# Optimization experiments

Hardware: AMD Instinct MI355X
Metric: run time of the kernel (lower is better)

## Reference

```python
import jax, jax.numpy as jnp
import numpy as np

# LinearMoELayer(input_size=2048, output_size=2048, num_experts=8, num_selects=2,
#                bias=True, gate_network='mlp', gate_use_balance=True,
#                gate_add_noise=True, gate_use_softmax=True)
# Eval-mode forward semantics (deterministic: noise branch only active in training).
B, S, D, O, E, K = 4, 2048, 2048, 2048, 8, 2
BAL_W = 1e-2   # balance_loss_weight
EPS = 1e-10    # cv_squared eps


def setup_inputs() -> dict:
    key = jax.random.key(0)
    ks = jax.random.split(key, 5)
    x = jax.random.normal(ks[0], (B, S, D), dtype=jnp.float32)
    # gate 'mlp': Linear(D,E,bias=False) -> tanh -> Linear(E,E,bias=False)
    gate_w1 = jax.random.normal(ks[1], (E, D), dtype=jnp.float32) * (1.0 / np.sqrt(D))
    gate_w2 = jax.random.normal(ks[2], (E, E), dtype=jnp.float32) * (1.0 / np.sqrt(E))
    # LinearExperts: per-expert weight [E, O, D] and bias [E, O] (F.linear convention)
    expert_w = jax.random.normal(ks[3], (E, O, D), dtype=jnp.float32) * (1.0 / np.sqrt(D))
    expert_b = jax.random.normal(ks[4], (E, O), dtype=jnp.float32) * 0.01
    return {"x": x, "gate_w1": gate_w1, "gate_w2": gate_w2,
            "expert_w": expert_w, "expert_b": expert_b}


def _cv_squared(v):
    # torch: v.var() / (v.mean()**2 + eps); torch.var is unbiased (ddof=1)
    m = jnp.mean(v)
    var = jnp.sum((v - m) ** 2) / (v.shape[0] - 1)
    return var / (m * m + EPS)


def reference(x, gate_w1, gate_w2, expert_w, expert_b):
    xt = x.reshape(-1, D)                                  # [T, D]
    T = xt.shape[0]
    # --- TopKBalancedNoisyGate (eval path) ---
    logits = jnp.tanh(xt @ gate_w1.T) @ gate_w2.T          # [T, E]
    top_logits, top_idx = jax.lax.top_k(logits, K)         # [T, K]
    scores = jax.nn.softmax(top_logits.astype(jnp.float32), axis=-1)  # [T, K]
    # scatter top-k scores into dense [T, E] gate matrix
    dense = jnp.zeros((T, E), dtype=scores.dtype)
    dense = dense.at[jnp.arange(T)[:, None], top_idx].set(scores)
    importance = dense.sum(axis=0)                         # [E]
    load = (dense > 0).sum(axis=0).astype(jnp.float32)     # [E] token counts
    gate_loss = BAL_W * (_cv_squared(importance) + _cv_squared(load))
    # --- UniversalCalculator: per-expert linear + score-weighted combine ---
    # math-equivalent to sort/dispatch/grouped-linear/index_add combine
    h = jnp.einsum('td,eod->teo', xt, expert_w) + expert_b[None, :, :]  # [T, E, O]
    y = jnp.einsum('te,teo->to', dense, h)                 # [T, O]
    return y.reshape(B, S, O), gate_loss
```

## Files before the change

kernel.cpp:

```cpp
#include <hip/hip_runtime.h>
#include <hip/hip_bf16.h>

#define TT 8192
#define DD 2048
#define OO 2048
#define EE 8

typedef __attribute__((ext_vector_type(4))) float f32x4;
typedef __attribute__((ext_vector_type(8))) short s16x8;
typedef __attribute__((ext_vector_type(4))) short s16x4;

__device__ __forceinline__ short f2bf(float f) {
    union { float f; unsigned u; } v; v.f = f;
    unsigned r = (v.u + 0x7FFFu + ((v.u >> 16) & 1u)) >> 16;
    return (short)(unsigned short)r;
}
__device__ __forceinline__ float bf2f(short s) {
    union { unsigned u; float f; } v; v.u = ((unsigned)(unsigned short)s) << 16;
    return v.f;
}

__global__ __launch_bounds__(256) void cvt_bf16_kernel(const float* __restrict__ in,
                                                       short* __restrict__ out, long n8) {
    long i = (long)blockIdx.x * blockDim.x + threadIdx.x;
    long stride = (long)gridDim.x * blockDim.x;
    for (; i < n8; i += stride) {
        f32x4 a = ((const f32x4*)in)[i * 2];
        f32x4 b = ((const f32x4*)in)[i * 2 + 1];
        s16x8 r;
        r[0] = f2bf(a[0]); r[1] = f2bf(a[1]); r[2] = f2bf(a[2]); r[3] = f2bf(a[3]);
        r[4] = f2bf(b[0]); r[5] = f2bf(b[1]); r[6] = f2bf(b[2]); r[7] = f2bf(b[3]);
        ((s16x8*)out)[i] = r;
    }
}

__global__ __launch_bounds__(256) void gate_kernel(
    const float* __restrict__ x, const float* __restrict__ w1, const float* __restrict__ w2,
    int* __restrict__ tk_idx, float* __restrict__ tk_score)
{
    const int lane = threadIdx.x & 63;
    const int wid = threadIdx.x >> 6;
    const int t = blockIdx.x * 4 + wid;
    const float* xt = x + (long)t * DD;

    float acc[8] = {0.f,0.f,0.f,0.f,0.f,0.f,0.f,0.f};
#pragma unroll
    for (int i = 0; i < DD / 256; ++i) {
        f32x4 xv = *(const f32x4*)&xt[i * 256 + lane * 4];
#pragma unroll
        for (int e2 = 0; e2 < 8; ++e2) {
            f32x4 wv = *(const f32x4*)&w1[e2 * DD + i * 256 + lane * 4];
            acc[e2] += xv[0]*wv[0] + xv[1]*wv[1] + xv[2]*wv[2] + xv[3]*wv[3];
        }
    }
#pragma unroll
    for (int e2 = 0; e2 < 8; ++e2) {
#pragma unroll
        for (int off = 32; off > 0; off >>= 1)
            acc[e2] += __shfl_xor(acc[e2], off, 64);
    }

    float th[8], lg[8];
#pragma unroll
    for (int e2 = 0; e2 < 8; ++e2) th[e2] = tanhf(acc[e2]);
#pragma unroll
    for (int eo = 0; eo < 8; ++eo) {
        float s = 0.f;
#pragma unroll
        for (int e2 = 0; e2 < 8; ++e2) s += th[e2] * w2[eo * 8 + e2];
        lg[eo] = s;
    }
    int e0 = 0;
#pragma unroll
    for (int q = 1; q < 8; ++q) if (lg[q] > lg[e0]) e0 = q;
    int e1 = (e0 == 0) ? 1 : 0;
#pragma unroll
    for (int q = 0; q < 8; ++q) if (q != e0 && lg[q] > lg[e1]) e1 = q;

    float d = expf(lg[e1] - lg[e0]);
    float s0 = 1.f / (1.f + d);
    float s1 = d / (1.f + d);

    if (lane == 0) {
        tk_idx[t * 2] = e0; tk_idx[t * 2 + 1] = e1;
        tk_score[t * 2] = s0; tk_score[t * 2 + 1] = s1;
    }
}

__global__ __launch_bounds__(256) void build_lists(
    const int* __restrict__ tk_idx, const float* __restrict__ tk_score,
    int* __restrict__ tok_list, float* __restrict__ score_list, int* __restrict__ cnt,
    float* __restrict__ imp)
{
    const int e = blockIdx.x;
    const int lane = threadIdx.x & 63;
    const int wid = threadIdx.x >> 6;
    __shared__ int wsum[4];
    __shared__ float wsumF[4];
    int base = 0;
    float ssum = 0.f;
    for (int t0 = 0; t0 < TT; t0 += 256) {
        int t = t0 + threadIdx.x;
        int i0 = tk_idx[t * 2], i1 = tk_idx[t * 2 + 1];
        bool has = (i0 == e) || (i1 == e);
        int slot = (i0 == e) ? 0 : 1;
        float sc = (i0 == e) ? tk_score[t * 2] : tk_score[t * 2 + 1];
        unsigned long long m = __ballot(has);
        int prefix = __popcll(m & ((1ull << lane) - 1ull));
        if (lane == 0) wsum[wid] = __popcll(m);
        __syncthreads();
        int woff = 0;
#pragma unroll
        for (int w = 0; w < 4; ++w) woff += (w < wid) ? wsum[w] : 0;
        int total = wsum[0] + wsum[1] + wsum[2] + wsum[3];
        if (has) {
            int p = base + woff + prefix;
            tok_list[e * TT + p] = t * 2 + slot;
            score_list[e * TT + p] = sc;
            ssum += sc;
        }
        base += total;
        __syncthreads();
    }
#pragma unroll
    for (int off = 32; off > 0; off >>= 1)
        ssum += __shfl_xor(ssum, off, 64);
    if (lane == 0) wsumF[wid] = ssum;
    __syncthreads();
    if (threadIdx.x == 0) {
        cnt[e] = base;
        imp[e] = wsumF[0] + wsumF[1] + wsumF[2] + wsumF[3];
    }
}

__global__ __launch_bounds__(64) void loss_finalize(const float* __restrict__ imp,
                                                    const int* __restrict__ cnt,
                                                    float* __restrict__ loss_out)
{
    if (threadIdx.x == 0) {
        float im[8], ld[8];
        float mi = 0.f, ml = 0.f;
#pragma unroll
        for (int q = 0; q < 8; ++q) {
            im[q] = imp[q]; ld[q] = (float)cnt[q];
            mi += im[q]; ml += ld[q];
        }
        mi *= 0.125f; ml *= 0.125f;
        float vi = 0.f, vl = 0.f;
#pragma unroll
        for (int q = 0; q < 8; ++q) {
            float a = im[q] - mi; vi += a * a;
            float b = ld[q] - ml; vl += b * b;
        }
        vi /= 7.f; vl /= 7.f;
        loss_out[0] = 0.01f * (vi / (mi * mi + 1e-10f) + vl / (ml * ml + 1e-10f));
    }
}

__global__ __launch_bounds__(256) void combine_kernel(float* __restrict__ y,
                                                      const short* __restrict__ part1) {
    long i = (long)blockIdx.x * blockDim.x + threadIdx.x;
    long stride = (long)gridDim.x * blockDim.x;
    const long n4 = (long)TT * OO / 4;
    for (; i < n4; i += stride) {
        f32x4 v = ((const f32x4*)y)[i];
        s16x4 p = ((const s16x4*)part1)[i];
        v[0] += bf2f(p[0]); v[1] += bf2f(p[1]);
        v[2] += bf2f(p[2]); v[3] += bf2f(p[3]);
        ((f32x4*)y)[i] = v;
    }
}

#define GLD16(gsrc, ldst) \
    __builtin_amdgcn_global_load_lds((const __attribute__((address_space(1))) unsigned int*)(gsrc), \
                                     (__attribute__((address_space(3))) unsigned int*)(ldst), 16, 0, 0)

#define BAR() __builtin_amdgcn_s_barrier()

__global__ __launch_bounds__(512, 2) void moe_gemm(
    const short* __restrict__ xbf, const short* __restrict__ wbf,
    const float* __restrict__ eb,
    const int* __restrict__ tok_list, const float* __restrict__ score_list,
    const int* __restrict__ cnt, float* __restrict__ y, short* __restrict__ part1)
{
    const int e = blockIdx.z;
    const int n_e = cnt[e];
    const int row0 = blockIdx.y * 256;
    if (row0 >= n_e) return;
    const int col0 = blockIdx.x * 256;

    __shared__ alignas(16) short lds[2 * 32768];
    __shared__ int   stok[256];
    __shared__ float ssc[256];

    const int tid = threadIdx.x;
    const int lane = tid & 63;
    const int wid = tid >> 6;
    const int wr = wid >> 2, wc = wid & 3;
    const int fr = lane & 15, fq = lane >> 4;
    const char* ldsb = (const char*)lds;

    if (tid < 256) {
        int slot = row0 + tid;
        if (slot >= n_e) slot = n_e - 1;
        stok[tid] = tok_list[e * TT + slot];
        ssc[tid]  = score_list[e * TT + slot];
    }
    __syncthreads();

    const int r_ = tid >> 3;
    const int csw = ((tid & 7) ^ (r_ & 7)) * 8;
    const short* aS[4];
#pragma unroll
    for (int g = 0; g < 4; ++g)
        aS[g] = xbf + (long)(stok[g * 64 + r_] >> 1) * DD + csw;
    const short* bS[4];
#pragma unroll
    for (int g = 0; g < 4; ++g)
        bS[g] = wbf + (long)e * OO * DD + (long)(col0 + g * 64 + r_) * DD + csw;

#define STAGE_A(g, kt) GLD16(aS[g] + (kt) * 64, (char*)lds + ((kt) & 1) * 65536 + ((g) * 512 + tid) * 16)
#define STAGE_B(g, kt) GLD16(bS[g] + (kt) * 64, (char*)lds + ((kt) & 1) * 65536 + 32768 + ((g) * 512 + tid) * 16)

    const int aBase = (wr * 128 + fr) * 128;
    const int bBase = 32768 + (wc * 64 + fr) * 128;
    const int sw0 = (fq ^ (fr & 7)) * 16;
    const int sw1 = ((fq + 4) ^ (fr & 7)) * 16;

    f32x4 acc[8][4];
#pragma unroll
    for (int m = 0; m < 8; ++m)
#pragma unroll
        for (int n = 0; n < 4; ++n) acc[m][n] = f32x4{0.f, 0.f, 0.f, 0.f};

    STAGE_A(0, 0); STAGE_A(1, 0); STAGE_A(2, 0); STAGE_A(3, 0);
    STAGE_B(0, 0); STAGE_B(1, 0); STAGE_B(2, 0); STAGE_B(3, 0);
    STAGE_A(0, 1); STAGE_A(1, 1);
    asm volatile("s_waitcnt vmcnt(2)");
    BAR();

#pragma unroll 1
    for (int j = 0; j < DD / 64; ++j) {
        const int fb = (j & 1) * 65536;
        const bool st1 = (j + 1) < DD / 64;
        const bool st2 = (j + 2) < DD / 64;

        s16x8 a0[4][2], a1[4][2], bb[4][2];

#pragma unroll
        for (int mm = 0; mm < 4; ++mm) {
            a0[mm][0] = *(const s16x8*)(ldsb + fb + aBase + mm * 2048 + sw0);
            a0[mm][1] = *(const s16x8*)(ldsb + fb + aBase + mm * 2048 + sw1);
        }
#pragma unroll
        for (int n = 0; n < 4; ++n) {
            bb[n][0] = *(const s16x8*)(ldsb + fb + bBase + n * 2048 + sw0);
            bb[n][1] = *(const s16x8*)(ldsb + fb + bBase + n * 2048 + sw1);
        }
        if (st1) {
            STAGE_A(2, j + 1); STAGE_A(3, j + 1);
            STAGE_B(0, j + 1); STAGE_B(1, j + 1);
            STAGE_B(2, j + 1); STAGE_B(3, j + 1);
        }
#pragma unroll
        for (int mm = 0; mm < 4; ++mm)
#pragma unroll
            for (int n = 0; n < 4; ++n) {
                acc[mm][n] = __builtin_amdgcn_mfma_f32_16x16x32_bf16(a0[mm][0], bb[n][0], acc[mm][n], 0, 0, 0);
                acc[mm][n] = __builtin_amdgcn_mfma_f32_16x16x32_bf16(a0[mm][1], bb[n][1], acc[mm][n], 0, 0, 0);
            }
#pragma unroll
        for (int mm = 0; mm < 4; ++mm) {
            a1[mm][0] = *(const s16x8*)(ldsb + fb + aBase + 8192 + mm * 2048 + sw0);
            a1[mm][1] = *(const s16x8*)(ldsb + fb + aBase + 8192 + mm * 2048 + sw1);
        }
#pragma unroll
        for (int mm = 0; mm < 4; ++mm)
#pragma unroll
            for (int n = 0; n < 4; ++n) {
                acc[4 + mm][n] = __builtin_amdgcn_mfma_f32_16x16x32_bf16(a1[mm][0], bb[n][0], acc[4 + mm][n], 0, 0, 0);
                acc[4 + mm][n] = __builtin_amdgcn_mfma_f32_16x16x32_bf16(a1[mm][1], bb[n][1], acc[4 + mm][n], 0, 0, 0);
            }

        BAR();
        if (st2) { STAGE_A(0, j + 2); STAGE_A(1, j + 2); }
        if (st2) { asm volatile("s_waitcnt vmcnt(2)"); }
        else     { asm volatile("s_waitcnt vmcnt(0)"); }
        BAR();
    }

    float bval[4];
#pragma unroll
    for (int n = 0; n < 4; ++n)
        bval[n] = eb[e * OO + col0 + wc * 64 + n * 16 + fr];

#pragma unroll
    for (int m = 0; m < 8; ++m) {
#pragma unroll
        for (int jj = 0; jj < 4; ++jj) {
            int tslot = wr * 128 + m * 16 + fq * 4 + jj;
            if (row0 + tslot < n_e) {
                int packed = stok[tslot];
                int t = packed >> 1;
                float s = ssc[tslot];
                if ((packed & 1) == 0) {
#pragma unroll
                    for (int n = 0; n < 4; ++n) {
                        int o = col0 + wc * 64 + n * 16 + fr;
                        y[(long)t * OO + o] = s * (acc[m][n][jj] + bval[n]);
                    }
                } else {
#pragma unroll
                    for (int n = 0; n < 4; ++n) {
                        int o = col0 + wc * 64 + n * 16 + fr;
                        part1[(long)t * OO + o] = f2bf(s * (acc[m][n][jj] + bval[n]));
                    }
                }
            }
        }
    }
#undef STAGE_A
#undef STAGE_B
}

extern "C" void kernel_launch(void* const* d_in, const int* in_sizes, int n_in,
                              void* d_out, int out_size, void* d_ws, size_t ws_size,
                              hipStream_t stream) {
    const float* x  = (const float*)d_in[0];
    const float* w1 = (const float*)d_in[1];
    const float* w2 = (const float*)d_in[2];
    const float* ew = (const float*)d_in[3];
    const float* eb = (const float*)d_in[4];
    float* y = (float*)d_out;

    char* ws = (char*)d_ws;
    short* xbf = (short*)ws;            ws += (size_t)TT * DD * 2;
    short* wbf = (short*)ws;            ws += (size_t)EE * OO * DD * 2;
    short* part1 = (short*)ws;          ws += (size_t)TT * OO * 2;
    int*   tok_list = (int*)ws;         ws += (size_t)EE * TT * 4;
    float* score_list = (float*)ws;     ws += (size_t)EE * TT * 4;
    int*   tk_idx = (int*)ws;           ws += (size_t)TT * 2 * 4;
    float* tk_score = (float*)ws;       ws += (size_t)TT * 2 * 4;
    int*   cnt = (int*)ws;              ws += 64;
    float* imp = (float*)ws;            ws += 64;

    cvt_bf16_kernel<<<4096, 256, 0, stream>>>(ew, wbf, (long)EE * OO * DD / 8);
    cvt_bf16_kernel<<<2048, 256, 0, stream>>>(x,  xbf, (long)TT * DD / 8);
    gate_kernel<<<TT / 4, 256, 0, stream>>>(x, w1, w2, tk_idx, tk_score);
    build_lists<<<EE, 256, 0, stream>>>(tk_idx, tk_score, tok_list, score_list, cnt, imp);
    loss_finalize<<<1, 64, 0, stream>>>(imp, cnt, y + (size_t)TT * OO);
    moe_gemm<<<dim3(OO / 256, TT / 256, EE), 512, 0, stream>>>(
        xbf, wbf, eb, tok_list, score_list, cnt, y, part1);
    combine_kernel<<<2048, 256, 0, stream>>>(y, part1);
}
```

Baseline: 333.5 us.

## Switch MoE GEMM to triple-buffered K=32 LDS pipeline with one barrier per step

Reworks the expert GEMM main loop from a double-buffered K=64 tile with two barriers per iteration into a three-stage ring of K=32 tiles. Each stage is prefetched two iterations ahead and a single barrier is issued per step. LDS use drops from 128KB to 96KB per block, and the swizzle is adjusted for 64-byte rows. The goal is deeper overlap of global-to-LDS loads with MFMA work and less barrier stall. The cost is twice as many loop iterations, with smaller per-iteration MFMA batches and more frequent waits.

```diff
diff --git a/kernel.cpp b/kernel.cpp
--- a/kernel.cpp
+++ b/kernel.cpp
@@ -189,7 +189,7 @@
     if (row0 >= n_e) return;
     const int col0 = blockIdx.x * 256;
 
-    __shared__ alignas(16) short lds[2 * 32768];
+    __shared__ alignas(16) short lds[3 * 16384];
     __shared__ int   stok[256];
     __shared__ float ssc[256];
 
@@ -208,24 +208,27 @@
     }
     __syncthreads();
 
-    const int r_ = tid >> 3;
-    const int csw = ((tid & 7) ^ (r_ & 7)) * 8;
-    const short* aS[4];
-#pragma unroll
-    for (int g = 0; g < 4; ++g)
-        aS[g] = xbf + (long)(stok[g * 64 + r_] >> 1) * DD + csw;
-    const short* bS[4];
-#pragma unroll
-    for (int g = 0; g < 4; ++g)
-        bS[g] = wbf + (long)e * OO * DD + (long)(col0 + g * 64 + r_) * DD + csw;
-
-#define STAGE_A(g, kt) GLD16(aS[g] + (kt) * 64, (char*)lds + ((kt) & 1) * 65536 + ((g) * 512 + tid) * 16)
-#define STAGE_B(g, kt) GLD16(bS[g] + (kt) * 64, (char*)lds + ((kt) & 1) * 65536 + 32768 + ((g) * 512 + tid) * 16)
-
-    const int aBase = (wr * 128 + fr) * 128;
-    const int bBase = 32768 + (wc * 64 + fr) * 128;
-    const int sw0 = (fq ^ (fr & 7)) * 16;
-    const int sw1 = ((fq + 4) ^ (fr & 7)) * 16;
+    const int r4 = tid >> 2;
+    const int csw = ((tid & 3) ^ (r4 & 3)) * 8;
+    const short* aS[2];
+#pragma unroll
+    for (int g = 0; g < 2; ++g)
+        aS[g] = xbf + (long)(stok[g * 128 + r4] >> 1) * DD + csw;
+    const short* bS[2];
+#pragma unroll
+    for (int g = 0; g < 2; ++g)
+        bS[g] = wbf + (long)e * OO * DD + (long)(col0 + g * 128 + r4) * DD + csw;
+
+#define STAGE(kt, fb2) do { \
+    GLD16(aS[0] + (kt) * 32, (char*)lds + (fb2) + tid * 16);                 \
+    GLD16(aS[1] + (kt) * 32, (char*)lds + (fb2) + 8192 + tid * 16);          \
+    GLD16(bS[0] + (kt) * 32, (char*)lds + (fb2) + 16384 + tid * 16);         \
+    GLD16(bS[1] + (kt) * 32, (char*)lds + (fb2) + 16384 + 8192 + tid * 16);  \
+} while (0)
+
+    const int aBase = (wr * 128 + fr) * 64;
+    const int bBase = 16384 + (wc * 64 + fr) * 64;
+    const int sw = (fq ^ (fr & 3)) * 16;
 
     f32x4 acc[8][4];
 #pragma unroll
@@ -233,60 +236,38 @@
 #pragma unroll
         for (int n = 0; n < 4; ++n) acc[m][n] = f32x4{0.f, 0.f, 0.f, 0.f};
 
-    STAGE_A(0, 0); STAGE_A(1, 0); STAGE_A(2, 0); STAGE_A(3, 0);
-    STAGE_B(0, 0); STAGE_B(1, 0); STAGE_B(2, 0); STAGE_B(3, 0);
-    STAGE_A(0, 1); STAGE_A(1, 1);
-    asm volatile("s_waitcnt vmcnt(2)");
+    STAGE(0, 0);
+    STAGE(1, 16384 * 2);
+    asm volatile("s_waitcnt vmcnt(4)");
     BAR();
 
+    int f = 0;
 #pragma unroll 1
-    for (int j = 0; j < DD / 64; ++j) {
-        const int fb = (j & 1) * 65536;
-        const bool st1 = (j + 1) < DD / 64;
-        const bool st2 = (j + 2) < DD / 64;
-
-        s16x8 a0[4][2], a1[4][2], bb[4][2];
-
-#pragma unroll
-        for (int mm = 0; mm < 4; ++mm) {
-            a0[mm][0] = *(const s16x8*)(ldsb + fb + aBase + mm * 2048 + sw0);
-            a0[mm][1] = *(const s16x8*)(ldsb + fb + aBase + mm * 2048 + sw1);
-        }
-#pragma unroll
-        for (int n = 0; n < 4; ++n) {
-            bb[n][0] = *(const s16x8*)(ldsb + fb + bBase + n * 2048 + sw0);
-            bb[n][1] = *(const s16x8*)(ldsb + fb + bBase + n * 2048 + sw1);
-        }
-        if (st1) {
-            STAGE_A(2, j + 1); STAGE_A(3, j + 1);
-            STAGE_B(0, j + 1); STAGE_B(1, j + 1);
-            STAGE_B(2, j + 1); STAGE_B(3, j + 1);
-        }
-#pragma unroll
-        for (int mm = 0; mm < 4; ++mm)
-#pragma unroll
-            for (int n = 0; n < 4; ++n) {
-                acc[mm][n] = __builtin_amdgcn_mfma_f32_16x16x32_bf16(a0[mm][0], bb[n][0], acc[mm][n], 0, 0, 0);
-                acc[mm][n] = __builtin_amdgcn_mfma_f32_16x16x32_bf16(a0[mm][1], bb[n][1], acc[mm][n], 0, 0, 0);
-            }
-#pragma unroll
-        for (int mm = 0; mm < 4; ++mm) {
-            a1[mm][0] = *(const s16x8*)(ldsb + fb + aBase + 8192 + mm * 2048 + sw0);
-            a1[mm][1] = *(const s16x8*)(ldsb + fb + aBase + 8192 + mm * 2048 + sw1);
-        }
-#pragma unroll
-        for (int mm = 0; mm < 4; ++mm)
-#pragma unroll
-            for (int n = 0; n < 4; ++n) {
-                acc[4 + mm][n] = __builtin_amdgcn_mfma_f32_16x16x32_bf16(a1[mm][0], bb[n][0], acc[4 + mm][n], 0, 0, 0);
-                acc[4 + mm][n] = __builtin_amdgcn_mfma_f32_16x16x32_bf16(a1[mm][1], bb[n][1], acc[4 + mm][n], 0, 0, 0);
-            }
-
-        BAR();
-        if (st2) { STAGE_A(0, j + 2); STAGE_A(1, j + 2); }
-        if (st2) { asm volatile("s_waitcnt vmcnt(2)"); }
+    for (int j = 0; j < DD / 32; ++j) {
+        const int fb = f * 32768;
+        const int f2 = (f + 2 >= 3) ? f - 1 : f + 2;
+        const bool st2 = (j + 2) < DD / 32;
+
+        if (st2) STAGE(j + 2, f2 * 32768);
+
+        s16x8 a[8], b[4];
+#pragma unroll
+        for (int m = 0; m < 8; ++m)
+            a[m] = *(const s16x8*)(ldsb + fb + aBase + m * 1024 + sw);
+#pragma unroll
+        for (int n = 0; n < 4; ++n)
+            b[n] = *(const s16x8*)(ldsb + fb + bBase + n * 1024 + sw);
+
+#pragma unroll
+        for (int m = 0; m < 8; ++m)
+#pragma unroll
+            for (int n = 0; n < 4; ++n)
+                acc[m][n] = __builtin_amdgcn_mfma_f32_16x16x32_bf16(a[m], b[n], acc[m][n], 0, 0, 0);
+
+        if (st2) { asm volatile("s_waitcnt vmcnt(4)"); }
         else     { asm volatile("s_waitcnt vmcnt(0)"); }
         BAR();
+        f = (f == 2) ? 0 : f + 1;
     }
 
     float bval[4];
@@ -319,8 +300,7 @@
             }
         }
     }
-#undef STAGE_A
-#undef STAGE_B
+#undef STAGE
 }
 
 extern "C" void kernel_launch(void* const* d_in, const int* in_sizes, int n_in,
```

Result: slower. 405.1 us (+21.5%).
